# Kernel tuning notes

Hardware: AMD Instinct MI355X
Metric: run time of the kernel (lower is better)

The kernel has to match this reference:

```python
import jax, jax.numpy as jnp
import numpy as np

L, N, DIN, DOUT = 24, 8192, 256, 128  # levels, nodes/level, dim_in(=2*dim_out), dim_out


def setup_inputs() -> dict:
    key = jax.random.key(0)
    ks = jax.random.split(key, 6)
    s = 1.0 / np.sqrt(DIN)
    tensor = jax.random.normal(ks[0], (L, N, DIN), jnp.float32)
    # child indices into previous level's nodes; -1 == missing child -> learned init state
    indices = jax.random.randint(ks[1], (L, N, 2), -1, N).astype(jnp.int32)
    W_w = jax.random.uniform(ks[2], (4 * DOUT, DIN), jnp.float32, -s, s)
    W_b = jax.random.uniform(ks[3], (4 * DOUT,), jnp.float32, -s, s)
    U_f1 = jax.random.uniform(ks[4], (DOUT, 2 * DOUT), jnp.float32, -s, s)
    U_f2 = jax.random.uniform(jax.random.fold_in(ks[4], 1), (DOUT, 2 * DOUT), jnp.float32, -s, s)
    U_iuo = jax.random.uniform(ks[5], (3 * DOUT, 2 * DOUT), jnp.float32, -s, s)
    h_init = jnp.zeros((1, DOUT), jnp.float32)
    c_init = jnp.zeros((1, DOUT), jnp.float32)
    return dict(tensor=tensor, indices=indices, h_init=h_init, c_init=c_init,
                W_w=W_w, W_b=W_b, U_f1=U_f1, U_f2=U_f2, U_iuo=U_iuo)


def reference(tensor, indices, h_init, c_init, W_w, W_b, U_f1, U_f2, U_iuo):
    D = DOUT

    def step(carry, inp):
        h_prev, c_prev = carry                      # [N, D] each (previous level)
        x, idx = inp                                # x:[N,DIN], idx:[N,2]
        h_ext = jnp.concatenate([h_init, h_prev], axis=0)  # row 0 = init (index -1)
        c_ext = jnp.concatenate([c_init, c_prev], axis=0)
        rows = idx + 1                              # -1 -> 0 (init state)
        h = h_ext[rows]                             # [N, 2, D] gathered child hiddens
        c = c_ext[rows]                             # [N, 2, D]
        W_x = x @ W_w.T + W_b                       # [N, 4D]
        f_x, i_x, u_x, o_x = jnp.split(W_x, 4, axis=1)
        hc = h.reshape(h.shape[0], 2 * D)           # [N, 2D]
        f1 = jax.nn.sigmoid(f_x + hc @ U_f1.T)
        f2 = jax.nn.sigmoid(f_x + hc @ U_f2.T)
        iuo = hc @ U_iuo.T                          # [N, 3D]
        i = jax.nn.sigmoid(iuo[:, :D] + i_x)
        u = jnp.tanh(iuo[:, D:2 * D] + u_x)
        o = jax.nn.sigmoid(iuo[:, 2 * D:] + o_x)
        new_c = i * u + f1 * c[:, 0] + f2 * c[:, 1]
        new_h = o * jnp.tanh(new_c)
        return (new_h, new_c), (new_h, new_c)

    n = tensor.shape[1]
    h0 = jnp.broadcast_to(h_init, (n, D))
    c0 = jnp.broadcast_to(c_init, (n, D))
    _, (res_h, res_c) = jax.lax.scan(step, (h0, c0), (tensor, indices))
    return res_h, res_c                              # each [L, N, D]
```

## Files before the change

### kernel.cpp

```cpp
#include <hip/hip_runtime.h>
#include <stdint.h>

#define LVL 24
#define NN  8192
#define DIN 256
#define DD  128
#define BM  32

typedef __attribute__((ext_vector_type(8))) short bf16x8;
typedef __attribute__((ext_vector_type(4))) float f32x4;

__device__ __forceinline__ float b2f(unsigned short u) {
    union { unsigned int i; float f; } v; v.i = ((unsigned int)u) << 16; return v.f;
}
__device__ __forceinline__ unsigned short f2b(float f) {
    union { float f; unsigned int i; } v; v.f = f;
    unsigned int x = v.i;
    return (unsigned short)((x + 0x7fffu + ((x >> 16) & 1u)) >> 16);
}
__device__ __forceinline__ float sig_(float x) { return 1.0f / (1.0f + __expf(-x)); }

__device__ __forceinline__ float ldf(const void* p, size_t i, int isf) {
    return isf ? ((const float*)p)[i] : b2f(((const unsigned short*)p)[i]);
}

__global__ void detect_kernel(const unsigned short* __restrict__ t, int* __restrict__ flag) {
    __shared__ int cnt;
    if (threadIdx.x == 0) cnt = 0;
    __syncthreads();
    int bad = 0;
    #pragma unroll
    for (int r = 0; r < 4; ++r) {
        unsigned short u = t[(threadIdx.x * 4 + r) * 2];
        int e = (u >> 7) & 255;
        bad += (e >= 136 || (e >= 1 && e <= 90)) ? 1 : 0;
    }
    atomicAdd(&cnt, bad);
    __syncthreads();
    if (threadIdx.x == 0) *flag = (cnt > 16) ? 1 : 0;
}

__global__ __launch_bounds__(256)
void convert_kernel(const void* Ww, const void* Wb, const void* Uf1, const void* Uf2,
                    const void* Uiuo, const void* hini, const void* cini,
                    unsigned short* __restrict__ wpack, float* __restrict__ bias,
                    unsigned short* __restrict__ hinit_b, float* __restrict__ cinit_f,
                    const int* __restrict__ flag) {
    const int isf = *flag;
    const int bid = blockIdx.x;
    const int t = threadIdx.x;
    if (bid < 1152) {
        const int row = bid, col = t;
        float v;
        if (row < 512)       v = ldf(Ww,   (size_t)row * DIN + col, isf);
        else if (row < 640)  v = ldf(Uf1,  (size_t)(row - 512) * DIN + col, isf);
        else if (row < 768)  v = ldf(Uf2,  (size_t)(row - 640) * DIN + col, isf);
        else                 v = ldf(Uiuo, (size_t)(row - 768) * DIN + col, isf);
        const int g  = row >> 7;
        const int wr = row & 127;
        const int dt = wr >> 4;
        const int mm = wr & 15;
        const int kk = col >> 5;
        const int q  = (col >> 3) & 3;
        const int j  = col & 7;
        const size_t pos = (size_t)((g * 8 + dt) * 8 + kk) * 512 + (q * 16 + mm) * 8 + j;
        wpack[pos] = f2b(v);
    } else if (bid == 1152) {
        bias[t] = ldf(Wb, t, isf);
    } else if (bid == 1153) {
        bias[256 + t] = ldf(Wb, 256 + t, isf);
    } else {
        if (t < 128) hinit_b[t] = f2b(ldf(hini, t, isf));
        else if (t < 256) cinit_f[t - 128] = ldf(cini, t - 128, isf);
    }
}

__global__ __launch_bounds__(256, 3)
void level_kernel(const void* __restrict__ xbase, int level,
                  const int* __restrict__ idx,
                  const unsigned short* __restrict__ hprev,
                  const float* __restrict__ cprev,
                  unsigned short* __restrict__ hnew,
                  float* __restrict__ outh,
                  float* __restrict__ outc,
                  const unsigned short* __restrict__ wpack,
                  const float* __restrict__ bias,
                  const unsigned short* __restrict__ hinit_b,
                  const float* __restrict__ cinit_f,
                  const int* __restrict__ flag,
                  int first) {
    __shared__ unsigned short xs[8192];
    __shared__ unsigned short hs[8192];
    __shared__ float cs[64 * 68];

    const int tid = threadIdx.x;
    const int isf = *flag;
    const int bm  = blockIdx.x;
    const int yh  = blockIdx.y;

    {
        const int u0 = tid >> 4;
        const int r0 = tid & 15;
        #pragma unroll
        for (int du = 0; du < 2; ++du) {
            const int u = u0 + du * 16;
            const int kk = u >> 2, q = u & 3;
            #pragma unroll
            for (int dr = 0; dr < 2; ++dr) {
                const int r = r0 + dr * 16;
                const size_t re = (size_t)level * NN * DIN + (size_t)(bm * BM + r) * DIN + u * 8;
                union { unsigned short us[8]; uint4 v; } t;
                if (isf) {
                    const float4* xr = (const float4*)((const float*)xbase + re);
                    float4 v0 = xr[0], v1 = xr[1];
                    t.us[0] = f2b(v0.x); t.us[1] = f2b(v0.y); t.us[2] = f2b(v0.z); t.us[3] = f2b(v0.w);
                    t.us[4] = f2b(v1.x); t.us[5] = f2b(v1.y); t.us[6] = f2b(v1.z); t.us[7] = f2b(v1.w);
                } else {
                    t.v = *(const uint4*)((const unsigned short*)xbase + re);
                }
                *(uint4*)&xs[kk * 1024 + q * 256 + r * 8] = t.v;
            }
        }
    }

    {
        const int r  = tid & 31;
        const int sp = tid >> 5;
        const int s    = sp >> 2;
        const int part = sp & 3;
        const int ai = idx[(bm * BM + r) * 2 + s];
        const int use_init = (first || ai < 0);

        const unsigned short* hsrc = use_init ? (hinit_b + part * 32)
                                              : (hprev + (size_t)ai * DD + part * 32);
        const int kk = s * 4 + part;
        #pragma unroll
        for (int q = 0; q < 4; ++q)
            *(uint4*)&hs[kk * 1024 + q * 256 + r * 8] = ((const uint4*)hsrc)[q];

        const float* csrc = use_init ? (cinit_f + yh * 64 + part * 16)
                                     : (cprev + (size_t)ai * DD + yh * 64 + part * 16);
        float* cdst = &cs[(s * 32 + r) * 68 + part * 16];
        #pragma unroll
        for (int q = 0; q < 4; ++q)
            ((float4*)cdst)[q] = ((const float4*)csrc)[q];
    }
    __syncthreads();

    const int lane = tid & 63;
    const int wave = tid >> 6;
    const int m    = lane & 15;
    const int q    = lane >> 4;
    const int dt   = yh * 4 + wave;
    const int d    = yh * 64 + wave * 16 + m;

    const unsigned short* wb = wpack + (size_t)dt * 4096 + (size_t)lane * 8;

    f32x4 acc[9][2];
    #pragma unroll
    for (int g = 0; g < 9; ++g) { acc[g][0] = (f32x4)0.0f; acc[g][1] = (f32x4)0.0f; }

    #pragma unroll
    for (int kk = 0; kk < 8; ++kk) {
        const int xo = kk * 1024 + q * 256 + m * 8;
        bf16x8 a0 = *(const bf16x8*)&xs[xo];
        bf16x8 a1 = *(const bf16x8*)&xs[xo + 128];
        bf16x8 h0 = *(const bf16x8*)&hs[xo];
        bf16x8 h1 = *(const bf16x8*)&hs[xo + 128];
        #pragma unroll
        for (int g = 0; g < 4; ++g) {
            bf16x8 b = *(const bf16x8*)(wb + (size_t)g * 32768 + kk * 512);
            acc[g][0] = __builtin_amdgcn_mfma_f32_16x16x32_bf16(a0, b, acc[g][0], 0, 0, 0);
            acc[g][1] = __builtin_amdgcn_mfma_f32_16x16x32_bf16(a1, b, acc[g][1], 0, 0, 0);
        }
        #pragma unroll
        for (int g = 4; g < 9; ++g) {
            bf16x8 b = *(const bf16x8*)(wb + (size_t)g * 32768 + kk * 512);
            acc[g][0] = __builtin_amdgcn_mfma_f32_16x16x32_bf16(h0, b, acc[g][0], 0, 0, 0);
            acc[g][1] = __builtin_amdgcn_mfma_f32_16x16x32_bf16(h1, b, acc[g][1], 0, 0, 0);
        }
    }

    const float bfv = bias[d], biv = bias[128 + d], buv = bias[256 + d], bov = bias[384 + d];
    const int dloc = wave * 16 + m;
    #pragma unroll
    for (int mt = 0; mt < 2; ++mt) {
        #pragma unroll
        for (int j = 0; j < 4; ++j) {
            const int rr = mt * 16 + q * 4 + j;
            const int nd = bm * BM + rr;
            const float ca = cs[rr * 68 + dloc];
            const float cb = cs[(32 + rr) * 68 + dloc];
            const float fx = acc[0][mt][j] + bfv;
            const float ix = acc[1][mt][j] + biv;
            const float ux = acc[2][mt][j] + buv;
            const float ox = acc[3][mt][j] + bov;
            const float f1 = sig_(fx + acc[4][mt][j]);
            const float f2 = sig_(fx + acc[5][mt][j]);
            const float ig = sig_(ix + acc[6][mt][j]);
            const float ug = tanhf(ux + acc[7][mt][j]);
            const float og = sig_(ox + acc[8][mt][j]);
            const float nc = ig * ug + f1 * ca + f2 * cb;
            const float nh = og * tanhf(nc);
            const size_t o = (size_t)nd * DD + d;
            hnew[o] = f2b(nh);
            outh[o] = nh;
            outc[o] = nc;
        }
    }
}

extern "C" void kernel_launch(void* const* d_in, const int* in_sizes, int n_in,
                              void* d_out, int out_size, void* d_ws, size_t ws_size,
                              hipStream_t stream) {
    const void* tensor  = d_in[0];
    const int*  indices = (const int*)d_in[1];
    const void* h_init  = d_in[2];
    const void* c_init  = d_in[3];
    const void* Ww      = d_in[4];
    const void* Wb      = d_in[5];
    const void* Uf1     = d_in[6];
    const void* Uf2     = d_in[7];
    const void* Uiuo    = d_in[8];
    float* out = (float*)d_out;

    char* wsb = (char*)d_ws;
    int* flag                = (int*)wsb;
    unsigned short* wpack    = (unsigned short*)(wsb + 256);
    float* bias              = (float*)(wsb + 590336);
    unsigned short* hinit_b  = (unsigned short*)(wsb + 592640);
    float* cinit_f           = (float*)(wsb + 593152);
    unsigned short* hb0      = (unsigned short*)(wsb + (1u << 20));
    unsigned short* hb1      = (unsigned short*)(wsb + (1u << 20) + 2097152);

    detect_kernel<<<1, 64, 0, stream>>>((const unsigned short*)tensor, flag);
    convert_kernel<<<1155, 256, 0, stream>>>(Ww, Wb, Uf1, Uf2, Uiuo, h_init, c_init,
                                             wpack, bias, hinit_b, cinit_f, flag);

    unsigned short* hp = hb0;
    unsigned short* hn = hb1;
    for (int l = 0; l < LVL; ++l) {
        const float* cprev = (l == 0) ? (const float*)out
                                      : (const float*)(out + (size_t)(LVL + l - 1) * NN * DD);
        level_kernel<<<dim3(NN / BM, 2), 256, 0, stream>>>(
            tensor, l,
            indices + (size_t)l * NN * 2,
            hp, cprev, hn,
            out + (size_t)l * NN * DD,
            out + (size_t)(LVL + l) * NN * DD,
            wpack, bias, hinit_b, cinit_f, flag, (l == 0) ? 1 : 0);
        unsigned short* th = hp; hp = hn; hn = th;
    }
}
```

Baseline: 747.9 us.

## Fuse all levels into one persistent cooperative kernel with a grid barrier

Replaces the 24 per-level launches with a single cooperative persistent kernel of 512 blocks. A hierarchical atomic barrier separates levels, and the next level's x tile is prefetched into a double-buffered shared-memory slot while the current level's epilogue runs. This is meant to remove per-launch overhead and the tail idle time between levels, and to overlap the x load with compute. In exchange it adds the spin-wait barrier cost, lowers occupancy to two blocks per CU through extra shared memory, and falls back to the old per-level path when co-residency is not possible.

```diff
diff --git a/kernel.cpp b/kernel.cpp
--- a/kernel.cpp
+++ b/kernel.cpp
@@ -6,6 +6,8 @@
 #define DIN 256
 #define DD  128
 #define BM  32
+#define NBLK 512
+#define CSW 66
 
 typedef __attribute__((ext_vector_type(8))) short bf16x8;
 typedef __attribute__((ext_vector_type(4))) float f32x4;
@@ -45,6 +47,7 @@
                     const void* Uiuo, const void* hini, const void* cini,
                     unsigned short* __restrict__ wpack, float* __restrict__ bias,
                     unsigned short* __restrict__ hinit_b, float* __restrict__ cinit_f,
+                    unsigned int* __restrict__ bar,
                     const int* __restrict__ flag) {
     const int isf = *flag;
     const int bid = blockIdx.x;
@@ -69,9 +72,189 @@
         bias[t] = ldf(Wb, t, isf);
     } else if (bid == 1153) {
         bias[256 + t] = ldf(Wb, 256 + t, isf);
-    } else {
+    } else if (bid == 1154) {
         if (t < 128) hinit_b[t] = f2b(ldf(hini, t, isf));
         else if (t < 256) cinit_f[t - 128] = ldf(cini, t - 128, isf);
+    } else {
+        for (int i = t; i < 320; i += 256) bar[i] = 0u;
+    }
+}
+
+__device__ __forceinline__ void stage_x_tile(unsigned short* __restrict__ xsbuf,
+                                             const void* __restrict__ xbase,
+                                             int level, int bm, int tid, int isf) {
+    const int u0 = tid >> 4;
+    const int r0 = tid & 15;
+    #pragma unroll
+    for (int du = 0; du < 2; ++du) {
+        const int u = u0 + du * 16;
+        const int kk = u >> 2, qq = u & 3;
+        #pragma unroll
+        for (int dr = 0; dr < 2; ++dr) {
+            const int r = r0 + dr * 16;
+            const size_t re = (size_t)level * NN * DIN + (size_t)(bm * BM + r) * DIN + u * 8;
+            union { unsigned short us[8]; uint4 v; } t;
+            if (isf) {
+                const float4* xr = (const float4*)((const float*)xbase + re);
+                float4 v0 = xr[0], v1 = xr[1];
+                t.us[0] = f2b(v0.x); t.us[1] = f2b(v0.y); t.us[2] = f2b(v0.z); t.us[3] = f2b(v0.w);
+                t.us[4] = f2b(v1.x); t.us[5] = f2b(v1.y); t.us[6] = f2b(v1.z); t.us[7] = f2b(v1.w);
+            } else {
+                t.v = *(const uint4*)((const unsigned short*)xbase + re);
+            }
+            *(uint4*)&xsbuf[kk * 1024 + qq * 256 + r * 8] = t.v;
+        }
+    }
+}
+
+__device__ __forceinline__ void lean_barrier(unsigned int* __restrict__ bar, int lvl, int bid) {
+    __syncthreads();
+    if (threadIdx.x == 0) {
+        __builtin_amdgcn_fence(__ATOMIC_RELEASE, "agent");
+        const int slot = bid & 7;
+        unsigned int prev = __hip_atomic_fetch_add(&bar[slot * 32], 1u,
+                                                   __ATOMIC_RELAXED, __HIP_MEMORY_SCOPE_AGENT);
+        if (prev + 1u == (unsigned int)(64 * (lvl + 1))) {
+            unsigned int mp = __hip_atomic_fetch_add(&bar[8 * 32], 1u,
+                                                     __ATOMIC_RELAXED, __HIP_MEMORY_SCOPE_AGENT);
+            if (mp + 1u == (unsigned int)(8 * (lvl + 1))) {
+                __hip_atomic_store(&bar[9 * 32], (unsigned int)(lvl + 1),
+                                   __ATOMIC_RELEASE, __HIP_MEMORY_SCOPE_AGENT);
+            }
+        }
+        while (__hip_atomic_load(&bar[9 * 32], __ATOMIC_RELAXED,
+                                 __HIP_MEMORY_SCOPE_AGENT) < (unsigned int)(lvl + 1))
+            __builtin_amdgcn_s_sleep(8);
+        __builtin_amdgcn_fence(__ATOMIC_ACQUIRE, "agent");
+    }
+    __syncthreads();
+}
+
+__global__ __launch_bounds__(256, 2)
+void fused_kernel(const void* __restrict__ xbase,
+                  const int* __restrict__ idxall,
+                  unsigned short* __restrict__ hb0,
+                  unsigned short* __restrict__ hb1,
+                  float* __restrict__ out,
+                  const unsigned short* __restrict__ wpack,
+                  const float* __restrict__ bias,
+                  const unsigned short* __restrict__ hinit_b,
+                  const float* __restrict__ cinit_f,
+                  const int* __restrict__ flag,
+                  unsigned int* __restrict__ bar) {
+    __shared__ unsigned short xs[2][8192];
+    __shared__ unsigned short hs[8192];
+    __shared__ float cs[64 * CSW];
+
+    const int tid = threadIdx.x;
+    const int isf = *flag;
+    const int bid = blockIdx.x;
+    const int bm  = bid & 255;
+    const int yh  = bid >> 8;
+
+    const int lane = tid & 63;
+    const int wave = tid >> 6;
+    const int m    = lane & 15;
+    const int q    = lane >> 4;
+    const int dt   = yh * 4 + wave;
+    const int d    = yh * 64 + wave * 16 + m;
+    const int dloc = wave * 16 + m;
+    const unsigned short* wb = wpack + (size_t)dt * 4096 + (size_t)lane * 8;
+    const float bfv = bias[d], biv = bias[128 + d], buv = bias[256 + d], bov = bias[384 + d];
+    const float ci_init = cinit_f[d];
+
+    const int gr  = tid & 31;
+    const int gsp = tid >> 5;
+    const int gs    = gsp >> 2;
+    const int gpart = gsp & 3;
+
+    stage_x_tile(xs[0], xbase, 0, bm, tid, isf);
+
+    for (int l = 0; l < LVL; ++l) {
+        const int first = (l == 0) ? 1 : 0;
+        const int* __restrict__ idx = idxall + (size_t)l * NN * 2;
+        const unsigned short* __restrict__ hprev = (l & 1) ? hb1 : hb0;
+        unsigned short* __restrict__ hnew        = (l & 1) ? hb0 : hb1;
+        const float* __restrict__ cprev = out + (size_t)(LVL + l - 1) * NN * DD;
+        float* __restrict__ outh = out + (size_t)l * NN * DD;
+        float* __restrict__ outc = out + (size_t)(LVL + l) * NN * DD;
+
+        {
+            const int ai = idx[(bm * BM + gr) * 2 + gs];
+            const int use_init = (first || ai < 0);
+
+            const unsigned short* hsrc = use_init ? (hinit_b + gpart * 32)
+                                                  : (hprev + (size_t)ai * DD + gpart * 32);
+            const int kk = gs * 4 + gpart;
+            #pragma unroll
+            for (int qq = 0; qq < 4; ++qq)
+                *(uint4*)&hs[kk * 1024 + qq * 256 + gr * 8] = ((const uint4*)hsrc)[qq];
+
+            const float* csrc = use_init ? (cinit_f + yh * 64 + gpart * 16)
+                                         : (cprev + (size_t)ai * DD + yh * 64 + gpart * 16);
+            float* cdst = &cs[(gs * 32 + gr) * CSW + gpart * 16];
+            #pragma unroll
+            for (int qq = 0; qq < 4; ++qq)
+                ((float4*)cdst)[qq] = ((const float4*)csrc)[qq];
+        }
+        __syncthreads();
+
+        const unsigned short* __restrict__ xcur = xs[l & 1];
+        f32x4 acc[9][2];
+        #pragma unroll
+        for (int g = 0; g < 9; ++g) { acc[g][0] = (f32x4)0.0f; acc[g][1] = (f32x4)0.0f; }
+
+        #pragma unroll
+        for (int kk = 0; kk < 8; ++kk) {
+            const int xo = kk * 1024 + q * 256 + m * 8;
+            bf16x8 a0 = *(const bf16x8*)&xcur[xo];
+            bf16x8 a1 = *(const bf16x8*)&xcur[xo + 128];
+            bf16x8 h0 = *(const bf16x8*)&hs[xo];
+            bf16x8 h1 = *(const bf16x8*)&hs[xo + 128];
+            #pragma unroll
+            for (int g = 0; g < 4; ++g) {
+                bf16x8 b = *(const bf16x8*)(wb + (size_t)g * 32768 + kk * 512);
+                acc[g][0] = __builtin_amdgcn_mfma_f32_16x16x32_bf16(a0, b, acc[g][0], 0, 0, 0);
+                acc[g][1] = __builtin_amdgcn_mfma_f32_16x16x32_bf16(a1, b, acc[g][1], 0, 0, 0);
+            }
+            #pragma unroll
+            for (int g = 4; g < 9; ++g) {
+                bf16x8 b = *(const bf16x8*)(wb + (size_t)g * 32768 + kk * 512);
+                acc[g][0] = __builtin_amdgcn_mfma_f32_16x16x32_bf16(h0, b, acc[g][0], 0, 0, 0);
+                acc[g][1] = __builtin_amdgcn_mfma_f32_16x16x32_bf16(h1, b, acc[g][1], 0, 0, 0);
+            }
+        }
+
+        if (l + 1 < LVL)
+            stage_x_tile(xs[(l + 1) & 1], xbase, l + 1, bm, tid, isf);
+
+        #pragma unroll
+        for (int mt = 0; mt < 2; ++mt) {
+            #pragma unroll
+            for (int j = 0; j < 4; ++j) {
+                const int rr = mt * 16 + q * 4 + j;
+                const int nd = bm * BM + rr;
+                const float ca = cs[rr * CSW + dloc];
+                const float cb = cs[(32 + rr) * CSW + dloc];
+                const float fx = acc[0][mt][j] + bfv;
+                const float ix = acc[1][mt][j] + biv;
+                const float ux = acc[2][mt][j] + buv;
+                const float ox = acc[3][mt][j] + bov;
+                const float f1 = sig_(fx + acc[4][mt][j]);
+                const float f2 = sig_(fx + acc[5][mt][j]);
+                const float ig = sig_(ix + acc[6][mt][j]);
+                const float ug = tanhf(ux + acc[7][mt][j]);
+                const float og = sig_(ox + acc[8][mt][j]);
+                const float nc = ig * ug + f1 * ca + f2 * cb;
+                const float nh = og * tanhf(nc);
+                const size_t o = (size_t)nd * DD + d;
+                hnew[o] = f2b(nh);
+                outh[o] = nh;
+                outc[o] = nc;
+            }
+        }
+
+        if (l + 1 < LVL) lean_barrier(bar, l, bid);
     }
 }
 
@@ -91,38 +274,14 @@
                   int first) {
     __shared__ unsigned short xs[8192];
     __shared__ unsigned short hs[8192];
-    __shared__ float cs[64 * 68];
+    __shared__ float cs[64 * CSW];
 
     const int tid = threadIdx.x;
     const int isf = *flag;
     const int bm  = blockIdx.x;
     const int yh  = blockIdx.y;
 
-    {
-        const int u0 = tid >> 4;
-        const int r0 = tid & 15;
-        #pragma unroll
-        for (int du = 0; du < 2; ++du) {
-            const int u = u0 + du * 16;
-            const int kk = u >> 2, q = u & 3;
-            #pragma unroll
-            for (int dr = 0; dr < 2; ++dr) {
-                const int r = r0 + dr * 16;
-                const size_t re = (size_t)level * NN * DIN + (size_t)(bm * BM + r) * DIN + u * 8;
-                union { unsigned short us[8]; uint4 v; } t;
-                if (isf) {
-                    const float4* xr = (const float4*)((const float*)xbase + re);
-                    float4 v0 = xr[0], v1 = xr[1];
-                    t.us[0] = f2b(v0.x); t.us[1] = f2b(v0.y); t.us[2] = f2b(v0.z); t.us[3] = f2b(v0.w);
-                    t.us[4] = f2b(v1.x); t.us[5] = f2b(v1.y); t.us[6] = f2b(v1.z); t.us[7] = f2b(v1.w);
-                } else {
-                    t.v = *(const uint4*)((const unsigned short*)xbase + re);
-                }
-                *(uint4*)&xs[kk * 1024 + q * 256 + r * 8] = t.v;
-            }
-        }
-    }
-
+    stage_x_tile(xs, xbase, level, bm, tid, isf);
     {
         const int r  = tid & 31;
         const int sp = tid >> 5;
@@ -135,15 +294,15 @@
                                               : (hprev + (size_t)ai * DD + part * 32);
         const int kk = s * 4 + part;
         #pragma unroll
-        for (int q = 0; q < 4; ++q)
-            *(uint4*)&hs[kk * 1024 + q * 256 + r * 8] = ((const uint4*)hsrc)[q];
+        for (int qq = 0; qq < 4; ++qq)
+            *(uint4*)&hs[kk * 1024 + qq * 256 + r * 8] = ((const uint4*)hsrc)[qq];
 
         const float* csrc = use_init ? (cinit_f + yh * 64 + part * 16)
                                      : (cprev + (size_t)ai * DD + yh * 64 + part * 16);
-        float* cdst = &cs[(s * 32 + r) * 68 + part * 16];
-        #pragma unroll
-        for (int q = 0; q < 4; ++q)
-            ((float4*)cdst)[q] = ((const float4*)csrc)[q];
+        float* cdst = &cs[(s * 32 + r) * CSW + part * 16];
+        #pragma unroll
+        for (int qq = 0; qq < 4; ++qq)
+            ((float4*)cdst)[qq] = ((const float4*)csrc)[qq];
     }
     __syncthreads();
 
@@ -153,7 +312,6 @@
     const int q    = lane >> 4;
     const int dt   = yh * 4 + wave;
     const int d    = yh * 64 + wave * 16 + m;
-
     const unsigned short* wb = wpack + (size_t)dt * 4096 + (size_t)lane * 8;
 
     f32x4 acc[9][2];
@@ -189,8 +347,8 @@
         for (int j = 0; j < 4; ++j) {
             const int rr = mt * 16 + q * 4 + j;
             const int nd = bm * BM + rr;
-            const float ca = cs[rr * 68 + dloc];
-            const float cb = cs[(32 + rr) * 68 + dloc];
+            const float ca = cs[rr * CSW + dloc];
+            const float cb = cs[(32 + rr) * CSW + dloc];
             const float fx = acc[0][mt][j] + bfv;
             const float ix = acc[1][mt][j] + biv;
             const float ux = acc[2][mt][j] + buv;
@@ -230,25 +388,40 @@
     float* bias              = (float*)(wsb + 590336);
     unsigned short* hinit_b  = (unsigned short*)(wsb + 592640);
     float* cinit_f           = (float*)(wsb + 593152);
+    unsigned int* bar        = (unsigned int*)(wsb + 594176);
     unsigned short* hb0      = (unsigned short*)(wsb + (1u << 20));
     unsigned short* hb1      = (unsigned short*)(wsb + (1u << 20) + 2097152);
 
     detect_kernel<<<1, 64, 0, stream>>>((const unsigned short*)tensor, flag);
-    convert_kernel<<<1155, 256, 0, stream>>>(Ww, Wb, Uf1, Uf2, Uiuo, h_init, c_init,
-                                             wpack, bias, hinit_b, cinit_f, flag);
-
-    unsigned short* hp = hb0;
-    unsigned short* hn = hb1;
-    for (int l = 0; l < LVL; ++l) {
-        const float* cprev = (l == 0) ? (const float*)out
-                                      : (const float*)(out + (size_t)(LVL + l - 1) * NN * DD);
-        level_kernel<<<dim3(NN / BM, 2), 256, 0, stream>>>(
-            tensor, l,
-            indices + (size_t)l * NN * 2,
-            hp, cprev, hn,
-            out + (size_t)l * NN * DD,
-            out + (size_t)(LVL + l) * NN * DD,
-            wpack, bias, hinit_b, cinit_f, flag, (l == 0) ? 1 : 0);
-        unsigned short* th = hp; hp = hn; hn = th;
-    }
-}
+    convert_kernel<<<1156, 256, 0, stream>>>(Ww, Wb, Uf1, Uf2, Uiuo, h_init, c_init,
+                                             wpack, bias, hinit_b, cinit_f, bar, flag);
+
+    static int nb = -1;
+    if (nb < 0) {
+        if (hipOccupancyMaxActiveBlocksPerMultiprocessor(&nb, fused_kernel, 256, 0)
+            != hipSuccess) nb = 0;
+    }
+
+    if (nb >= 2) {
+        void* kargs[] = { (void*)&tensor, (void*)&indices, (void*)&hb0, (void*)&hb1,
+                          (void*)&out, (void*)&wpack, (void*)&bias, (void*)&hinit_b,
+                          (void*)&cinit_f, (void*)&flag, (void*)&bar };
+        hipLaunchCooperativeKernel((const void*)fused_kernel, dim3(NBLK), dim3(256),
+                                   kargs, 0, stream);
+    } else {
+        unsigned short* hp = hb0;
+        unsigned short* hn = hb1;
+        for (int l = 0; l < LVL; ++l) {
+            const float* cprev = (l == 0) ? (const float*)out
+                                          : (const float*)(out + (size_t)(LVL + l - 1) * NN * DD);
+            level_kernel<<<dim3(NN / BM, 2), 256, 0, stream>>>(
+                tensor, l,
+                indices + (size_t)l * NN * 2,
+                hp, cprev, hn,
+                out + (size_t)l * NN * DD,
+                out + (size_t)(LVL + l) * NN * DD,
+                wpack, bias, hinit_b, cinit_f, flag, (l == 0) ? 1 : 0);
+            unsigned short* th = hp; hp = hn; hn = th;
+        }
+    }
+}
```

Result: no change. 751.7 us (+0.5%).

## Merge the two D-half blocks into one 512-thread block and use fast tanh

Applied to the files above, without the earlier changes.

Each block now has 8 waves and covers all 128 output columns for its 32 rows, replacing two 256-thread blocks that each handled 64 columns. The x tile and gathered child h rows are loaded and converted once per row block instead of twice, and the c tile is widened to the full row. tanhf is replaced with an exp-based tanh to make the epilogue cheaper, which can overflow to inf/inf (NaN) for large inputs. Launch bounds change to 512 threads, minimum 4 blocks, which tightens the register budget.

```diff
diff --git a/kernel.cpp b/kernel.cpp
--- a/kernel.cpp
+++ b/kernel.cpp
@@ -6,6 +6,7 @@
 #define DIN 256
 #define DD  128
 #define BM  32
+#define CSW 132
 
 typedef __attribute__((ext_vector_type(8))) short bf16x8;
 typedef __attribute__((ext_vector_type(4))) float f32x4;
@@ -19,6 +20,10 @@
     return (unsigned short)((x + 0x7fffu + ((x >> 16) & 1u)) >> 16);
 }
 __device__ __forceinline__ float sig_(float x) { return 1.0f / (1.0f + __expf(-x)); }
+__device__ __forceinline__ float tanh_(float x) {
+    float e = __expf(2.0f * x);
+    return (e - 1.0f) / (e + 1.0f);
+}
 
 __device__ __forceinline__ float ldf(const void* p, size_t i, int isf) {
     return isf ? ((const float*)p)[i] : b2f(((const unsigned short*)p)[i]);
@@ -75,7 +80,7 @@
     }
 }
 
-__global__ __launch_bounds__(256, 3)
+__global__ __launch_bounds__(512, 4)
 void level_kernel(const void* __restrict__ xbase, int level,
                   const int* __restrict__ idx,
                   const unsigned short* __restrict__ hprev,
@@ -91,68 +96,63 @@
                   int first) {
     __shared__ unsigned short xs[8192];
     __shared__ unsigned short hs[8192];
-    __shared__ float cs[64 * 68];
+    __shared__ float cs[64 * CSW];
 
     const int tid = threadIdx.x;
     const int isf = *flag;
     const int bm  = blockIdx.x;
-    const int yh  = blockIdx.y;
+
+    const int gr = tid & 31;
+    const int gs = (tid >> 5) & 1;
+    const int p2 = tid >> 6;
+    const int ai = idx[(bm * BM + gr) * 2 + gs];
+    const int use_init = (first || ai < 0);
 
     {
-        const int u0 = tid >> 4;
-        const int r0 = tid & 15;
+        const int r  = tid & 31;
+        const int u0 = tid >> 5;
         #pragma unroll
         for (int du = 0; du < 2; ++du) {
             const int u = u0 + du * 16;
-            const int kk = u >> 2, q = u & 3;
-            #pragma unroll
-            for (int dr = 0; dr < 2; ++dr) {
-                const int r = r0 + dr * 16;
-                const size_t re = (size_t)level * NN * DIN + (size_t)(bm * BM + r) * DIN + u * 8;
-                union { unsigned short us[8]; uint4 v; } t;
-                if (isf) {
-                    const float4* xr = (const float4*)((const float*)xbase + re);
-                    float4 v0 = xr[0], v1 = xr[1];
-                    t.us[0] = f2b(v0.x); t.us[1] = f2b(v0.y); t.us[2] = f2b(v0.z); t.us[3] = f2b(v0.w);
-                    t.us[4] = f2b(v1.x); t.us[5] = f2b(v1.y); t.us[6] = f2b(v1.z); t.us[7] = f2b(v1.w);
-                } else {
-                    t.v = *(const uint4*)((const unsigned short*)xbase + re);
-                }
-                *(uint4*)&xs[kk * 1024 + q * 256 + r * 8] = t.v;
+            const int kk = u >> 2, qq = u & 3;
+            const size_t re = (size_t)level * NN * DIN + (size_t)(bm * BM + r) * DIN + u * 8;
+            union { unsigned short us[8]; uint4 v; } t;
+            if (isf) {
+                const float4* xr = (const float4*)((const float*)xbase + re);
+                float4 v0 = xr[0], v1 = xr[1];
+                t.us[0] = f2b(v0.x); t.us[1] = f2b(v0.y); t.us[2] = f2b(v0.z); t.us[3] = f2b(v0.w);
+                t.us[4] = f2b(v1.x); t.us[5] = f2b(v1.y); t.us[6] = f2b(v1.z); t.us[7] = f2b(v1.w);
+            } else {
+                t.v = *(const uint4*)((const unsigned short*)xbase + re);
             }
+            *(uint4*)&xs[kk * 1024 + qq * 256 + r * 8] = t.v;
         }
     }
 
     {
-        const int r  = tid & 31;
-        const int sp = tid >> 5;
-        const int s    = sp >> 2;
-        const int part = sp & 3;
-        const int ai = idx[(bm * BM + r) * 2 + s];
-        const int use_init = (first || ai < 0);
-
-        const unsigned short* hsrc = use_init ? (hinit_b + part * 32)
-                                              : (hprev + (size_t)ai * DD + part * 32);
-        const int kk = s * 4 + part;
-        #pragma unroll
-        for (int q = 0; q < 4; ++q)
-            *(uint4*)&hs[kk * 1024 + q * 256 + r * 8] = ((const uint4*)hsrc)[q];
-
-        const float* csrc = use_init ? (cinit_f + yh * 64 + part * 16)
-                                     : (cprev + (size_t)ai * DD + yh * 64 + part * 16);
-        float* cdst = &cs[(s * 32 + r) * 68 + part * 16];
-        #pragma unroll
-        for (int q = 0; q < 4; ++q)
-            ((float4*)cdst)[q] = ((const float4*)csrc)[q];
+        const unsigned short* hrow = use_init ? hinit_b : (hprev + (size_t)ai * DD);
+        #pragma unroll
+        for (int i = 0; i < 2; ++i) {
+            const int cc = p2 * 2 + i;
+            const int kk = gs * 4 + (cc >> 2);
+            const int qq = cc & 3;
+            *(uint4*)&hs[kk * 1024 + qq * 256 + gr * 8] = *(const uint4*)(hrow + cc * 8);
+        }
+        const float* crow = use_init ? cinit_f : (cprev + (size_t)ai * DD);
+        float* cdst = &cs[(gs * 32 + gr) * CSW];
+        #pragma unroll
+        for (int i = 0; i < 4; ++i) {
+            const int cf = p2 * 4 + i;
+            *(float4*)(cdst + cf * 4) = *(const float4*)(crow + cf * 4);
+        }
     }
     __syncthreads();
 
     const int lane = tid & 63;
-    const int wave = tid >> 6;
+    const int dt   = tid >> 6;
     const int m    = lane & 15;
     const int q    = lane >> 4;
-    const int dt   = yh * 4 + wave;
-    const int d    = yh * 64 + wave * 16 + m;
+    const int d    = dt * 16 + m;
 
     const unsigned short* wb = wpack + (size_t)dt * 4096 + (size_t)lane * 8;
 
@@ -182,15 +182,14 @@
     }
 
     const float bfv = bias[d], biv = bias[128 + d], buv = bias[256 + d], bov = bias[384 + d];
-    const int dloc = wave * 16 + m;
     #pragma unroll
     for (int mt = 0; mt < 2; ++mt) {
         #pragma unroll
         for (int j = 0; j < 4; ++j) {
             const int rr = mt * 16 + q * 4 + j;
             const int nd = bm * BM + rr;
-            const float ca = cs[rr * 68 + dloc];
-            const float cb = cs[(32 + rr) * 68 + dloc];
+            const float ca = cs[rr * CSW + d];
+            const float cb = cs[(32 + rr) * CSW + d];
             const float fx = acc[0][mt][j] + bfv;
             const float ix = acc[1][mt][j] + biv;
             const float ux = acc[2][mt][j] + buv;
@@ -198,10 +197,10 @@
             const float f1 = sig_(fx + acc[4][mt][j]);
             const float f2 = sig_(fx + acc[5][mt][j]);
             const float ig = sig_(ix + acc[6][mt][j]);
-            const float ug = tanhf(ux + acc[7][mt][j]);
+            const float ug = tanh_(ux + acc[7][mt][j]);
             const float og = sig_(ox + acc[8][mt][j]);
             const float nc = ig * ug + f1 * ca + f2 * cb;
-            const float nh = og * tanhf(nc);
+            const float nh = og * tanh_(nc);
             const size_t o = (size_t)nd * DD + d;
             hnew[o] = f2b(nh);
             outh[o] = nh;
@@ -242,7 +241,7 @@
     for (int l = 0; l < LVL; ++l) {
         const float* cprev = (l == 0) ? (const float*)out
                                       : (const float*)(out + (size_t)(LVL + l - 1) * NN * DD);
-        level_kernel<<<dim3(NN / BM, 2), 256, 0, stream>>>(
+        level_kernel<<<NN / BM, 512, 0, stream>>>(
             tensor, l,
             indices + (size_t)l * NN * 2,
             hp, cprev, hn,
```

New measurement: 890.6 us. +19.1%, slower.
